# Performance work log

Hardware: AMD Instinct MI355X
Metric: run time of the kernel (lower is better)

## Reference

```python
import jax, jax.numpy as jnp
import numpy as np

L1 = 512
LX = 32
COUNT = 8


def setup_inputs() -> dict:
    key = jax.random.key(0)
    ks = jax.random.split(key, 9)
    B = 65536
    x = jax.random.uniform(ks[0], (B, 2 * L1), dtype=jnp.float32)  # NNUE accumulator is in [0,1]
    ls_indices = jax.random.randint(ks[1], (B,), 0, COUNT, dtype=jnp.int64)
    # params (scaled ~1/sqrt(fan_in))
    w_fact = jax.random.normal(ks[2], (LX, 2 * L1), dtype=jnp.float32) * (1.0 / np.sqrt(2 * L1))
    w0 = jax.random.normal(ks[3], (LX * COUNT, 2 * L1), dtype=jnp.float32) * (1.0 / np.sqrt(2 * L1))
    b0 = jax.random.normal(ks[4], (LX * COUNT,), dtype=jnp.float32) * 0.05
    w1 = jax.random.normal(ks[5], (LX * COUNT, LX), dtype=jnp.float32) * (1.0 / np.sqrt(LX))
    b1 = jax.random.normal(ks[6], (LX * COUNT,), dtype=jnp.float32) * 0.05
    w2 = jax.random.normal(ks[7], (1 * COUNT, LX), dtype=jnp.float32) * (1.0 / np.sqrt(LX))
    b2 = jax.random.normal(ks[8], (1 * COUNT,), dtype=jnp.float32) * 0.05
    return {"x": x, "ls_indices": ls_indices, "w_fact": w_fact,
            "w0": w0, "b0": b0, "w1": w1, "b1": b1, "w2": w2, "b2": b2}


def _stack_linear_gather(h, w, b, idx, out_dim):
    # dense Linear for all COUNT buckets, then gather the selected bucket per row
    y = (h @ w.T + b).reshape(-1, COUNT, out_dim)          # [B, COUNT, out_dim]
    return y.reshape(-1, out_dim)[idx]                      # [B, out_dim]


def reference(x, ls_indices, w_fact, w0, b0, w1, b1, w2, b2):
    B = x.shape[0]
    idx = ls_indices.astype(jnp.int32) + jnp.arange(B, dtype=jnp.int32) * COUNT
    l1f = x @ w_fact.T                                      # [B, LX]
    h = _stack_linear_gather(x, w0, b0, idx, LX) + l1f      # layer 0 + factorized term
    h = jnp.clip(h, 0.0, 1.0)
    h = _stack_linear_gather(h, w1, b1, idx, LX)            # hidden layer 1
    h = jnp.clip(h, 0.0, 1.0)
    out = _stack_linear_gather(h, w2, b2, idx, 1)           # output layer (no clamp)
    return out
```

## Files before the change

kernel.cpp:

```cpp
#include <hip/hip_runtime.h>


#define B_ROWS 65536
#define LK     1024
#define TILE   32
#define NBLK   (B_ROWS / TILE)


typedef short  short8  __attribute__((ext_vector_type(8)));
typedef float  f32x16  __attribute__((ext_vector_type(16)));

__device__ __forceinline__ unsigned pkbf(float a, float b) {
    unsigned ua = __float_as_uint(a), ub = __float_as_uint(b);
    ua = (ua + 0x7FFFu + ((ua >> 16) & 1u)) >> 16;
    ub = (ub + 0x7FFFu + ((ub >> 16) & 1u)) >> 16;
    return (ua & 0xFFFFu) | (ub << 16);
}

__device__ __forceinline__ unsigned cvtpk(float a, float b) {
    unsigned r;
    asm("v_cvt_pk_bf16_f32 %0, %1, %2" : "=v"(r) : "v"(a), "v"(b));
    return r;
}

__device__ __forceinline__ bool detect_i64(const int* p) {
    int acc = 0;
#pragma unroll
    for (int i = 0; i < 64; ++i) acc |= p[2 * i + 1];
    return acc == 0;
}

__device__ __forceinline__ int load_bucket(const int* p, int r, bool i64) {
    return (i64 ? p[2 * r] : p[r]) & 7;
}

__global__ __launch_bounds__(1024) void k_prep(
    const float* __restrict__ w0, const float* __restrict__ wf,
    uint4* __restrict__ wB)
{
    int f = blockIdx.x * 1024 + threadIdx.x;
    int b   = f >> 12;
    int i12 = f & 4095;
    int kc  = i12 >> 8;
    int i8  = i12 & 255;
    int n   = i8 & 31;
    int khi = i8 >> 5;
    int k = kc * 64 + khi * 8;
    const float* p0 = w0 + (size_t)(b * 32 + n) * LK + k;
    const float* pf = wf + (size_t)n * LK + k;
    float v[8];
#pragma unroll
    for (int j = 0; j < 8; ++j) v[j] = p0[j] + pf[j];
    uint4 o;
    o.x = pkbf(v[0], v[1]); o.y = pkbf(v[2], v[3]);
    o.z = pkbf(v[4], v[5]); o.w = pkbf(v[6], v[7]);
    wB[f] = o;
}

__global__ __launch_bounds__(256, 4) void k_main(
    const float* __restrict__ x, const int* __restrict__ idx,
    const uint4* __restrict__ wB, const float* __restrict__ b0,
    const float* __restrict__ w1, const float* __restrict__ b1,
    const float* __restrict__ w2, const float* __restrict__ b2,
    float* __restrict__ out)
{
    __shared__ float hb[TILE * 36];
    __shared__ int   bkt_s[TILE];

    int row0 = blockIdx.x * TILE;
    int t    = threadIdx.x;
    int lane = t & 63;
    int wv   = t >> 6;

    if (t < TILE) {
        bool i64 = detect_i64(idx);
        bkt_s[t] = load_bucket(idx, row0 + t, i64);
    }
    __syncthreads();

    const uint4* wB0 = wB + (size_t)(2 * wv) * 4096;
    const uint4* wB1 = wB0 + 4096;
    const float* Ab  = x + (size_t)(row0 + (lane & 31)) * LK + (lane >> 5) * 8;

    f32x16 acc0, acc1;
#pragma unroll
    for (int i = 0; i < 16; ++i) { acc0[i] = 0.0f; acc1[i] = 0.0f; }

    union UA { uint4 u; short8 s; };
    union UB { uint4 u; short8 s; };
#pragma unroll 4
    for (int c = 0; c < 64; ++c) {
        float4 a0 = *(const float4*)(Ab + c * 16);
        float4 a1 = *(const float4*)(Ab + c * 16 + 4);
        UB ub0, ub1;
        ub0.u = wB0[c * 64 + lane];
        ub1.u = wB1[c * 64 + lane];
        UA ua;
        ua.u.x = cvtpk(a0.x, a0.y);
        ua.u.y = cvtpk(a0.z, a0.w);
        ua.u.z = cvtpk(a1.x, a1.y);
        ua.u.w = cvtpk(a1.z, a1.w);
        acc0 = __builtin_amdgcn_mfma_f32_32x32x16_bf16(ua.s, ub0.s, acc0, 0, 0, 0);
        acc1 = __builtin_amdgcn_mfma_f32_32x32x16_bf16(ua.s, ub1.s, acc1, 0, 0, 0);
    }

    int bb0 = 2 * wv, bb1 = 2 * wv + 1;
#pragma unroll
    for (int i = 0; i < 16; ++i) {
        int m = (i & 3) + 8 * (i >> 2) + 4 * (lane >> 5);
        int n = lane & 31;
        int mb = bkt_s[m];
        if (mb == bb0 || mb == bb1) {
            float s = (mb == bb0) ? acc0[i] : acc1[i];
            float h = s + b0[mb * 32 + n];
            hb[m * 36 + n] = fminf(fmaxf(h, 0.0f), 1.0f);
        }
    }
    __syncthreads();

    if (t < 64) {
        int r = t >> 1, half = t & 1;
        int bkt = bkt_s[r];
        const float4* hr = (const float4*)(hb + r * 36);
        float4 ha[8];
#pragma unroll
        for (int q = 0; q < 8; ++q) ha[q] = hr[q];
        const float* w1b = w1 + (size_t)bkt * 1024;
        const float* b1b = b1 + bkt * 32;
        const float* w2b = w2 + bkt * 32;
        float partial = 0.0f;
#pragma unroll
        for (int jj = 0; jj < 16; ++jj) {
            int j2 = half * 16 + jj;
            const float4* wr = (const float4*)&w1b[j2 * 32];
            float s = b1b[j2];
#pragma unroll
            for (int q = 0; q < 8; ++q) {
                float4 w4 = wr[q];
                s += ha[q].x * w4.x + ha[q].y * w4.y + ha[q].z * w4.z + ha[q].w * w4.w;
            }
            s = fminf(fmaxf(s, 0.0f), 1.0f);
            partial += s * w2b[j2];
        }
        partial += __shfl_xor(partial, 1);
        if (half == 0) out[row0 + r] = partial + b2[bkt];
    }
}

extern "C" void kernel_launch(void* const* d_in, const int* in_sizes, int n_in,
                              void* d_out, int out_size, void* d_ws, size_t ws_size,
                              hipStream_t stream) {
    const float* x   = (const float*)d_in[0];
    const int*   lsi = (const int*)  d_in[1];
    const float* wf  = (const float*)d_in[2];
    const float* w0  = (const float*)d_in[3];
    const float* b0  = (const float*)d_in[4];
    const float* w1  = (const float*)d_in[5];
    const float* b1  = (const float*)d_in[6];
    const float* w2  = (const float*)d_in[7];
    const float* b2  = (const float*)d_in[8];
    float* out = (float*)d_out;

    uint4* wB = (uint4*)d_ws;

    k_prep<<<32, 1024, 0, stream>>>(w0, wf, wB);
    k_main<<<NBLK, 256, 0, stream>>>(x, lsi, wB, b0, w1, b1, w2, b2, out);
}
```

Before: 513.3 us.

## Stage x tile through double-buffered LDS as bf16 shared by all waves

```diff
diff --git a/kernel.cpp b/kernel.cpp
--- a/kernel.cpp
+++ b/kernel.cpp
@@ -5,6 +5,9 @@
 #define LK     1024
 #define TILE   32
 #define NBLK   (B_ROWS / TILE)
+#define KC     256
+#define NCH    (LK / KC)
+#define SROW   520
 
 
 typedef short  short8  __attribute__((ext_vector_type(8)));
@@ -64,6 +67,7 @@
     const float* __restrict__ w2, const float* __restrict__ b2,
     float* __restrict__ out)
 {
+    __shared__ __align__(16) unsigned char a_s[2 * TILE * SROW];
     __shared__ float hb[TILE * 36];
     __shared__ int   bkt_s[TILE];
 
@@ -76,32 +80,64 @@
         bool i64 = detect_i64(idx);
         bkt_s[t] = load_bucket(idx, row0 + t, i64);
     }
+
+    const float4* gsrc = (const float4*)(x + (size_t)(row0 + (t >> 6)) * LK)
+                         + (t & 63);
+    const int wb_off = (t >> 6) * SROW + (t & 63) * 8;
+
+    float4 v[8];
+#pragma unroll
+    for (int q = 0; q < 8; ++q) v[q] = gsrc[q * 1024];
+#pragma unroll
+    for (int q = 0; q < 8; ++q) {
+        uint2 o; o.x = cvtpk(v[q].x, v[q].y); o.y = cvtpk(v[q].z, v[q].w);
+        *(uint2*)(a_s + wb_off + q * 4 * SROW) = o;
+    }
     __syncthreads();
 
     const uint4* wB0 = wB + (size_t)(2 * wv) * 4096;
     const uint4* wB1 = wB0 + 4096;
-    const float* Ab  = x + (size_t)(row0 + (lane & 31)) * LK + (lane >> 5) * 8;
 
     f32x16 acc0, acc1;
 #pragma unroll
     for (int i = 0; i < 16; ++i) { acc0[i] = 0.0f; acc1[i] = 0.0f; }
 
-    union UA { uint4 u; short8 s; };
-    union UB { uint4 u; short8 s; };
-#pragma unroll 4
-    for (int c = 0; c < 64; ++c) {
-        float4 a0 = *(const float4*)(Ab + c * 16);
-        float4 a1 = *(const float4*)(Ab + c * 16 + 4);
-        UB ub0, ub1;
-        ub0.u = wB0[c * 64 + lane];
-        ub1.u = wB1[c * 64 + lane];
-        UA ua;
-        ua.u.x = cvtpk(a0.x, a0.y);
-        ua.u.y = cvtpk(a0.z, a0.w);
-        ua.u.z = cvtpk(a1.x, a1.y);
-        ua.u.w = cvtpk(a1.z, a1.w);
-        acc0 = __builtin_amdgcn_mfma_f32_32x32x16_bf16(ua.s, ub0.s, acc0, 0, 0, 0);
-        acc1 = __builtin_amdgcn_mfma_f32_32x32x16_bf16(ua.s, ub1.s, acc1, 0, 0, 0);
+    union UA { uint2 h[2]; short8 s; };
+    union UB { uint4 u;    short8 s; };
+
+    for (int ck = 0; ck < NCH; ++ck) {
+        const unsigned char* cur = a_s + (ck & 1) * (TILE * SROW);
+        unsigned char* nxt = a_s + ((ck + 1) & 1) * (TILE * SROW);
+        bool pf = (ck + 1 < NCH);
+
+        if (pf) {
+#pragma unroll
+            for (int q = 0; q < 8; ++q) v[q] = gsrc[(ck + 1) * 64 + q * 1024];
+        }
+
+        const unsigned char* Ab = cur + (size_t)(lane & 31) * SROW
+                                      + 16 * (lane >> 5);
+#pragma unroll
+        for (int cc = 0; cc < 16; ++cc) {
+            int c = ck * 16 + cc;
+            UA ua;
+            ua.h[0] = *(const uint2*)(Ab + 32 * cc);
+            ua.h[1] = *(const uint2*)(Ab + 32 * cc + 8);
+            UB ub0, ub1;
+            ub0.u = wB0[c * 64 + lane];
+            ub1.u = wB1[c * 64 + lane];
+            acc0 = __builtin_amdgcn_mfma_f32_32x32x16_bf16(ua.s, ub0.s, acc0, 0, 0, 0);
+            acc1 = __builtin_amdgcn_mfma_f32_32x32x16_bf16(ua.s, ub1.s, acc1, 0, 0, 0);
+        }
+
+        if (pf) {
+#pragma unroll
+            for (int q = 0; q < 8; ++q) {
+                uint2 o; o.x = cvtpk(v[q].x, v[q].y); o.y = cvtpk(v[q].z, v[q].w);
+                *(uint2*)(nxt + wb_off + q * 4 * SROW) = o;
+            }
+        }
+        __syncthreads();
     }
 
     int bb0 = 2 * wv, bb1 = 2 * wv + 1;
```

New measurement: 417.3 us. 1.23x faster.

## Group rows by bucket and compute only selected-bucket MFMA tiles

Applied to the files above, without the earlier changes.

```diff
diff --git a/kernel.cpp b/kernel.cpp
--- a/kernel.cpp
+++ b/kernel.cpp
@@ -3,9 +3,15 @@
 
 #define B_ROWS 65536
 #define LK     1024
-#define TILE   32
-#define NBLK   (B_ROWS / TILE)
-
+#define ROWS   64
+#define NBLK   (B_ROWS / ROWS)
+#define KC     64
+#define NCH    (LK / KC)
+#define SROW   136
+#define BUFSZ  (ROWS * SROW)
+#define MAXNT  9
+
+#define BKT_OFF 524288
 
 typedef short  short8  __attribute__((ext_vector_type(8)));
 typedef float  f32x16  __attribute__((ext_vector_type(16)));
@@ -35,10 +41,22 @@
 }
 
 __global__ __launch_bounds__(1024) void k_prep(
-    const float* __restrict__ w0, const float* __restrict__ wf,
-    uint4* __restrict__ wB)
+    const int* __restrict__ idx, const float* __restrict__ w0,
+    const float* __restrict__ wf, uint4* __restrict__ wB,
+    unsigned char* __restrict__ bktg)
 {
-    int f = blockIdx.x * 1024 + threadIdx.x;
+    int t = threadIdx.x;
+    if (blockIdx.x == 32) {
+        __shared__ int s_i64;
+        if (t == 0) s_i64 = detect_i64(idx) ? 1 : 0;
+        __syncthreads();
+        bool i64 = (s_i64 != 0);
+#pragma unroll 4
+        for (int j = 0; j < 64; ++j)
+            bktg[j * 1024 + t] = (unsigned char)load_bucket(idx, j * 1024 + t, i64);
+        return;
+    }
+    int f = blockIdx.x * 1024 + t;
     int b   = f >> 12;
     int i12 = f & 4095;
     int kc  = i12 >> 8;
@@ -58,68 +76,140 @@
 }
 
 __global__ __launch_bounds__(256, 4) void k_main(
-    const float* __restrict__ x, const int* __restrict__ idx,
+    const float* __restrict__ x, const unsigned char* __restrict__ bktg,
     const uint4* __restrict__ wB, const float* __restrict__ b0,
     const float* __restrict__ w1, const float* __restrict__ b1,
     const float* __restrict__ w2, const float* __restrict__ b2,
     float* __restrict__ out)
 {
-    __shared__ float hb[TILE * 36];
-    __shared__ int   bkt_s[TILE];
-
-    int row0 = blockIdx.x * TILE;
+    __shared__ __align__(16) unsigned char a_s[2 * BUFSZ];
+    __shared__ int bkt_s[ROWS];
+    __shared__ unsigned short order[ROWS];
+    __shared__ int cnt8[8], cur8[8];
+    __shared__ int tb_b[MAXNT], tb_s0[MAXNT], tb_l[MAXNT];
+    __shared__ int NT_s;
+
+    float* hb = (float*)a_s;
+
+    int row0 = blockIdx.x * ROWS;
     int t    = threadIdx.x;
     int lane = t & 63;
     int wv   = t >> 6;
-
-    if (t < TILE) {
-        bool i64 = detect_i64(idx);
-        bkt_s[t] = load_bucket(idx, row0 + t, i64);
-    }
-    __syncthreads();
-
-    const uint4* wB0 = wB + (size_t)(2 * wv) * 4096;
-    const uint4* wB1 = wB0 + 4096;
-    const float* Ab  = x + (size_t)(row0 + (lane & 31)) * LK + (lane >> 5) * 8;
-
-    f32x16 acc0, acc1;
-#pragma unroll
-    for (int i = 0; i < 16; ++i) { acc0[i] = 0.0f; acc1[i] = 0.0f; }
-
-    union UA { uint4 u; short8 s; };
-    union UB { uint4 u; short8 s; };
-#pragma unroll 4
-    for (int c = 0; c < 64; ++c) {
-        float4 a0 = *(const float4*)(Ab + c * 16);
-        float4 a1 = *(const float4*)(Ab + c * 16 + 4);
-        UB ub0, ub1;
-        ub0.u = wB0[c * 64 + lane];
-        ub1.u = wB1[c * 64 + lane];
-        UA ua;
-        ua.u.x = cvtpk(a0.x, a0.y);
-        ua.u.y = cvtpk(a0.z, a0.w);
-        ua.u.z = cvtpk(a1.x, a1.y);
-        ua.u.w = cvtpk(a1.z, a1.w);
-        acc0 = __builtin_amdgcn_mfma_f32_32x32x16_bf16(ua.s, ub0.s, acc0, 0, 0, 0);
-        acc1 = __builtin_amdgcn_mfma_f32_32x32x16_bf16(ua.s, ub1.s, acc1, 0, 0, 0);
-    }
-
-    int bb0 = 2 * wv, bb1 = 2 * wv + 1;
-#pragma unroll
-    for (int i = 0; i < 16; ++i) {
-        int m = (i & 3) + 8 * (i >> 2) + 4 * (lane >> 5);
-        int n = lane & 31;
-        int mb = bkt_s[m];
-        if (mb == bb0 || mb == bb1) {
-            float s = (mb == bb0) ? acc0[i] : acc1[i];
-            float h = s + b0[mb * 32 + n];
-            hb[m * 36 + n] = fminf(fmaxf(h, 0.0f), 1.0f);
-        }
-    }
-    __syncthreads();
-
-    if (t < 64) {
-        int r = t >> 1, half = t & 1;
+    int hi   = lane >> 5;
+    int nn   = lane & 31;
+
+    const float4* gp = (const float4*)x + (size_t)(row0 + (t >> 4)) * 256 + (t & 15);
+    float4 v[4];
+#pragma unroll
+    for (int q = 0; q < 4; ++q) v[q] = gp[q * 4096];
+
+    if (t < 8) cnt8[t] = 0;
+    __syncthreads();
+    int myb = 0;
+    if (t < ROWS) {
+        myb = (int)bktg[row0 + t];
+        bkt_s[t] = myb;
+        atomicAdd(&cnt8[myb], 1);
+    }
+    __syncthreads();
+    if (t == 0) {
+        int base = 0, nt = 0;
+        for (int b = 0; b < 8; ++b) {
+            int n = cnt8[b];
+            cur8[b] = base;
+            for (int j = 0; j < n; j += 32) {
+                tb_b[nt] = b; tb_s0[nt] = base + j; tb_l[nt] = min(32, n - j);
+                nt++;
+            }
+            base += n;
+        }
+        NT_s = nt;
+    }
+    __syncthreads();
+    if (t < ROWS) {
+        int pos = atomicAdd(&cur8[myb], 1);
+        order[pos] = (unsigned short)t;
+    }
+
+    const int wb_off = (t >> 4) * SROW + (t & 15) * 8;
+#pragma unroll
+    for (int q = 0; q < 4; ++q) {
+        uint2 o; o.x = cvtpk(v[q].x, v[q].y); o.y = cvtpk(v[q].z, v[q].w);
+        *(uint2*)(a_s + wb_off + q * 16 * SROW) = o;
+    }
+    __syncthreads();
+
+    int NT = NT_s;
+    int vs[3], sl[3], ss[3], aoff[3];
+    const uint4* wp[3];
+    float b0v[3];
+    f32x16 acc[3];
+#pragma unroll
+    for (int s = 0; s < 3; ++s) {
+        int tau = wv + 4 * s;
+        int val = (tau < NT) ? 1 : 0;
+        int b  = val ? tb_b[tau]  : 0;
+        int st = val ? tb_s0[tau] : 0;
+        int ln = val ? tb_l[tau]  : 0;
+        int rr = (nn < ln) ? (int)order[st + nn] : 0;
+        vs[s] = val; sl[s] = ln; ss[s] = st;
+        aoff[s] = rr * SROW + 16 * hi;
+        wp[s]   = wB + (size_t)b * 4096 + lane;
+        b0v[s]  = b0[b * 32 + nn];
+#pragma unroll
+        for (int i = 0; i < 16; ++i) acc[s][i] = 0.0f;
+    }
+
+    union UAB { uint4 u; short8 s8; };
+    for (int ck = 0; ck < NCH; ++ck) {
+        const unsigned char* cur = a_s + (ck & 1) * BUFSZ;
+        unsigned char* nxt = a_s + ((ck + 1) & 1) * BUFSZ;
+        if (ck + 1 < NCH) {
+#pragma unroll
+            for (int q = 0; q < 4; ++q) v[q] = gp[q * 4096 + (ck + 1) * 16];
+        }
+#pragma unroll
+        for (int s = 0; s < 3; ++s) {
+            if (vs[s]) {
+#pragma unroll
+                for (int cc = 0; cc < 4; ++cc) {
+                    UAB ua, ub;
+                    ua.u = *(const uint4*)(cur + aoff[s] + 32 * cc);
+                    ub.u = wp[s][(4 * ck + cc) * 64];
+                    acc[s] = __builtin_amdgcn_mfma_f32_32x32x16_bf16(
+                                 ua.s8, ub.s8, acc[s], 0, 0, 0);
+                }
+            }
+        }
+        if (ck + 1 < NCH) {
+#pragma unroll
+            for (int q = 0; q < 4; ++q) {
+                uint2 o; o.x = cvtpk(v[q].x, v[q].y); o.y = cvtpk(v[q].z, v[q].w);
+                *(uint2*)(nxt + wb_off + q * 16 * SROW) = o;
+            }
+        }
+        __syncthreads();
+    }
+
+#pragma unroll
+    for (int s = 0; s < 3; ++s) {
+        if (vs[s]) {
+#pragma unroll
+            for (int i = 0; i < 16; ++i) {
+                int m = (i & 3) + 8 * (i >> 2) + 4 * hi;
+                if (m < sl[s]) {
+                    int r = (int)order[ss[s] + m];
+                    float h = acc[s][i] + b0v[s];
+                    hb[r * 36 + nn] = fminf(fmaxf(h, 0.0f), 1.0f);
+                }
+            }
+        }
+    }
+    __syncthreads();
+
+    {
+        int r  = t >> 2;
+        int qt = t & 3;
         int bkt = bkt_s[r];
         const float4* hr = (const float4*)(hb + r * 36);
         float4 ha[8];
@@ -130,8 +220,8 @@
         const float* w2b = w2 + bkt * 32;
         float partial = 0.0f;
 #pragma unroll
-        for (int jj = 0; jj < 16; ++jj) {
-            int j2 = half * 16 + jj;
+        for (int jj = 0; jj < 8; ++jj) {
+            int j2 = qt * 8 + jj;
             const float4* wr = (const float4*)&w1b[j2 * 32];
             float s = b1b[j2];
 #pragma unroll
@@ -143,7 +233,8 @@
             partial += s * w2b[j2];
         }
         partial += __shfl_xor(partial, 1);
-        if (half == 0) out[row0 + r] = partial + b2[bkt];
+        partial += __shfl_xor(partial, 2);
+        if (qt == 0) out[row0 + r] = partial + b2[bkt];
     }
 }
 
@@ -161,8 +252,10 @@
     const float* b2  = (const float*)d_in[8];
     float* out = (float*)d_out;
 
-    uint4* wB = (uint4*)d_ws;
-
-    k_prep<<<32, 1024, 0, stream>>>(w0, wf, wB);
-    k_main<<<NBLK, 256, 0, stream>>>(x, lsi, wB, b0, w1, b1, w2, b2, out);
-}
+    char* ws = (char*)d_ws;
+    uint4* wB = (uint4*)ws;
+    unsigned char* bktg = (unsigned char*)(ws + BKT_OFF);
+
+    k_prep<<<33, 1024, 0, stream>>>(lsi, w0, wf, wB, bktg);
+    k_main<<<NBLK, 256, 0, stream>>>(x, bktg, wB, b0, w1, b1, w2, b2, out);
+}
```

After: 437.6 us. -14.8%, faster.

## Stage x tile through double-buffered LDS as bf16 and precompute buckets in prep

Applied to the files above, without the earlier changes.

```diff
diff --git a/kernel.cpp b/kernel.cpp
--- a/kernel.cpp
+++ b/kernel.cpp
@@ -5,7 +5,12 @@
 #define LK     1024
 #define TILE   32
 #define NBLK   (B_ROWS / TILE)
-
+#define KC     128
+#define NCH    (LK / KC)
+#define SROW   264
+#define BUFSZ  (TILE * SROW)
+
+#define BKT_OFF 524288
 
 typedef short  short8  __attribute__((ext_vector_type(8)));
 typedef float  f32x16  __attribute__((ext_vector_type(16)));
@@ -35,10 +40,22 @@
 }
 
 __global__ __launch_bounds__(1024) void k_prep(
-    const float* __restrict__ w0, const float* __restrict__ wf,
-    uint4* __restrict__ wB)
+    const int* __restrict__ idx, const float* __restrict__ w0,
+    const float* __restrict__ wf, uint4* __restrict__ wB,
+    unsigned char* __restrict__ bktg)
 {
-    int f = blockIdx.x * 1024 + threadIdx.x;
+    int t = threadIdx.x;
+    if (blockIdx.x == 32) {
+        __shared__ int s_i64;
+        if (t == 0) s_i64 = detect_i64(idx) ? 1 : 0;
+        __syncthreads();
+        bool i64 = (s_i64 != 0);
+#pragma unroll 4
+        for (int j = 0; j < 64; ++j)
+            bktg[j * 1024 + t] = (unsigned char)load_bucket(idx, j * 1024 + t, i64);
+        return;
+    }
+    int f = blockIdx.x * 1024 + t;
     int b   = f >> 12;
     int i12 = f & 4095;
     int kc  = i12 >> 8;
@@ -57,13 +74,14 @@
     wB[f] = o;
 }
 
-__global__ __launch_bounds__(256, 4) void k_main(
-    const float* __restrict__ x, const int* __restrict__ idx,
+__global__ __launch_bounds__(256, 3) void k_main(
+    const float* __restrict__ x, const unsigned char* __restrict__ bktg,
     const uint4* __restrict__ wB, const float* __restrict__ b0,
     const float* __restrict__ w1, const float* __restrict__ b1,
     const float* __restrict__ w2, const float* __restrict__ b2,
     float* __restrict__ out)
 {
+    __shared__ __align__(16) unsigned char a_s[2 * BUFSZ];
     __shared__ float hb[TILE * 36];
     __shared__ int   bkt_s[TILE];
 
@@ -71,49 +89,76 @@
     int t    = threadIdx.x;
     int lane = t & 63;
     int wv   = t >> 6;
-
-    if (t < TILE) {
-        bool i64 = detect_i64(idx);
-        bkt_s[t] = load_bucket(idx, row0 + t, i64);
+    int hi   = lane >> 5;
+    int nn   = lane & 31;
+
+    if (t < TILE) bkt_s[t] = (int)bktg[row0 + t];
+
+    const float4* gp = (const float4*)x + (size_t)(row0 + (t >> 5)) * 256 + (t & 31);
+    const int wb_off = (t >> 5) * SROW + (t & 31) * 8;
+
+    float4 v[4];
+#pragma unroll
+    for (int q = 0; q < 4; ++q) v[q] = gp[q * 2048];
+#pragma unroll
+    for (int q = 0; q < 4; ++q) {
+        uint2 o; o.x = cvtpk(v[q].x, v[q].y); o.y = cvtpk(v[q].z, v[q].w);
+        *(uint2*)(a_s + wb_off + q * 8 * SROW) = o;
     }
     __syncthreads();
 
-    const uint4* wB0 = wB + (size_t)(2 * wv) * 4096;
+    const uint4* wB0 = wB + (size_t)(2 * wv) * 4096 + lane;
     const uint4* wB1 = wB0 + 4096;
-    const float* Ab  = x + (size_t)(row0 + (lane & 31)) * LK + (lane >> 5) * 8;
 
     f32x16 acc0, acc1;
 #pragma unroll
     for (int i = 0; i < 16; ++i) { acc0[i] = 0.0f; acc1[i] = 0.0f; }
 
-    union UA { uint4 u; short8 s; };
-    union UB { uint4 u; short8 s; };
-#pragma unroll 4
-    for (int c = 0; c < 64; ++c) {
-        float4 a0 = *(const float4*)(Ab + c * 16);
-        float4 a1 = *(const float4*)(Ab + c * 16 + 4);
-        UB ub0, ub1;
-        ub0.u = wB0[c * 64 + lane];
-        ub1.u = wB1[c * 64 + lane];
-        UA ua;
-        ua.u.x = cvtpk(a0.x, a0.y);
-        ua.u.y = cvtpk(a0.z, a0.w);
-        ua.u.z = cvtpk(a1.x, a1.y);
-        ua.u.w = cvtpk(a1.z, a1.w);
-        acc0 = __builtin_amdgcn_mfma_f32_32x32x16_bf16(ua.s, ub0.s, acc0, 0, 0, 0);
-        acc1 = __builtin_amdgcn_mfma_f32_32x32x16_bf16(ua.s, ub1.s, acc1, 0, 0, 0);
+    union UAB { uint4 u; short8 s8; };
+
+    for (int ck = 0; ck < NCH; ++ck) {
+        const unsigned char* cur = a_s + (ck & 1) * BUFSZ;
+        unsigned char* nxt = a_s + ((ck + 1) & 1) * BUFSZ;
+
+        UAB w0r[8], w1r[8];
+#pragma unroll
+        for (int cc = 0; cc < 8; ++cc) w0r[cc].u = wB0[(ck * 8 + cc) * 64];
+#pragma unroll
+        for (int cc = 0; cc < 8; ++cc) w1r[cc].u = wB1[(ck * 8 + cc) * 64];
+
+        if (ck + 1 < NCH) {
+#pragma unroll
+            for (int q = 0; q < 4; ++q) v[q] = gp[q * 2048 + (ck + 1) * 32];
+        }
+
+        const unsigned char* Ab = cur + (size_t)(lane & 31) * SROW + 16 * hi;
+#pragma unroll
+        for (int cc = 0; cc < 8; ++cc) {
+            UAB ua;
+            ua.u = *(const uint4*)(Ab + 32 * cc);
+            acc0 = __builtin_amdgcn_mfma_f32_32x32x16_bf16(ua.s8, w0r[cc].s8, acc0, 0, 0, 0);
+            acc1 = __builtin_amdgcn_mfma_f32_32x32x16_bf16(ua.s8, w1r[cc].s8, acc1, 0, 0, 0);
+        }
+
+        if (ck + 1 < NCH) {
+#pragma unroll
+            for (int q = 0; q < 4; ++q) {
+                uint2 o; o.x = cvtpk(v[q].x, v[q].y); o.y = cvtpk(v[q].z, v[q].w);
+                *(uint2*)(nxt + wb_off + q * 8 * SROW) = o;
+            }
+        }
+        __syncthreads();
     }
 
     int bb0 = 2 * wv, bb1 = 2 * wv + 1;
 #pragma unroll
     for (int i = 0; i < 16; ++i) {
-        int m = (i & 3) + 8 * (i >> 2) + 4 * (lane >> 5);
-        int n = lane & 31;
+        int m = (i & 3) + 8 * (i >> 2) + 4 * hi;
         int mb = bkt_s[m];
         if (mb == bb0 || mb == bb1) {
             float s = (mb == bb0) ? acc0[i] : acc1[i];
-            float h = s + b0[mb * 32 + n];
-            hb[m * 36 + n] = fminf(fmaxf(h, 0.0f), 1.0f);
+            float h = s + b0[mb * 32 + nn];
+            hb[m * 36 + nn] = fminf(fmaxf(h, 0.0f), 1.0f);
         }
     }
     __syncthreads();
@@ -161,8 +206,10 @@
     const float* b2  = (const float*)d_in[8];
     float* out = (float*)d_out;
 
-    uint4* wB = (uint4*)d_ws;
-
-    k_prep<<<32, 1024, 0, stream>>>(w0, wf, wB);
-    k_main<<<NBLK, 256, 0, stream>>>(x, lsi, wB, b0, w1, b1, w2, b2, out);
-}
+    char* ws = (char*)d_ws;
+    uint4* wB = (uint4*)ws;
+    unsigned char* bktg = (unsigned char*)(ws + BKT_OFF);
+
+    k_prep<<<33, 1024, 0, stream>>>(lsi, w0, wf, wB, bktg);
+    k_main<<<NBLK, 256, 0, stream>>>(x, bktg, wB, b0, w1, b1, w2, b2, out);
+}
```

After: 417.8 us. 18.6% less time.
